# Performance work log

Measured on AMD Instinct MI355X. Metric: run time of the kernel, lower is better.

Reference implementation:

```python
import jax, jax.numpy as jnp
import numpy as np

B, D_IN, D_SAE = 4096, 1024, 16384
K_TOTAL = 262144  # B * 64 average active latents per sample


def setup_inputs() -> dict:
    key = jax.random.key(0)
    k1, k2, k3 = jax.random.split(key, 3)
    x = jax.random.normal(k1, (B, D_IN), dtype=jnp.float32)
    # torch kaiming_uniform_(a=sqrt(5)) on Linear weight -> bound = 1/sqrt(fan_in)
    bound_enc = 1.0 / np.sqrt(D_IN)
    W_enc = jax.random.uniform(k2, (D_IN, D_SAE), jnp.float32, -bound_enc, bound_enc)
    b_enc = jnp.zeros((D_SAE,), jnp.float32)
    bound_dec = 1.0 / np.sqrt(D_SAE)
    W_dec = jax.random.uniform(k3, (D_SAE, D_IN), jnp.float32, -bound_dec, bound_dec)
    b_dec = jnp.zeros((D_IN,), jnp.float32)
    return {"x": x, "W_enc": W_enc, "b_enc": b_enc,
            "W_dec": W_dec, "b_dec": b_dec, "k_total": K_TOTAL}


def reference(x, W_enc, b_enc, W_dec, b_dec, k_total):
    # encode: relu(x @ W_enc + b_enc), a: [B, M]
    a = jax.nn.relu(x @ W_enc + b_enc)
    Bn, M = a.shape
    # global batch top-k over the flattened activations, scatter back to sparse z
    flat = a.reshape(-1)                          # [B*M]
    vals, idx = jax.lax.top_k(flat, k_total)      # k_total is a static Python int
    z = jnp.zeros_like(flat).at[idx].set(vals).reshape(Bn, M)
    # decode
    x_hat = z @ W_dec + b_dec                     # [B, D_IN]
    # metrics (detached in torch; plain values here)
    nnz = (z > 0).sum()
    frac_nnz = nnz.astype(jnp.float32) / (Bn * M)
    mean_active = z.sum() / jnp.maximum(nnz.astype(jnp.float32), 1.0)
    return x_hat, z, frac_nnz, mean_active, nnz
```

## Files before the change

### kernel.cpp

```cpp
#include <hip/hip_runtime.h>
#include <stdint.h>

#define D_IN 1024
#define M_SAE 16384
#define NROWS 4096
#define NTOT 67108864
#define K_TOTAL 262144

#define META_OFF    0
#define GHIST_OFF   4096
#define ROWCNT_OFF  69632
#define PSUM_OFF    86016
#define CAND_OFF    102400
#define CAND_CAP    1048576
#define CAND2_OFF   8491008
#define CAND2_CAP   32768
#define ROWLIST_OFF 8753152
#define ROW_CAP     256
#define XBF_OFF     17141760
#define WBT_OFF     25530368

#define HBASE 7872u
#define HBINS 512
#define F_BITS 0x3FB00000u
#define FBIN   8152u
#define CBUF_CAP 1024

typedef __bf16 bf16x8 __attribute__((ext_vector_type(8)));
typedef float  f32x4  __attribute__((ext_vector_type(4)));

__device__ __forceinline__ unsigned short f2bf(float f) {
    uint32_t u = __float_as_uint(f);
    uint32_t r = u + 0x7FFFu + ((u >> 16) & 1u);
    return (unsigned short)(r >> 16);
}
__device__ __forceinline__ float bf2f(unsigned short s) {
    return __uint_as_float(((uint32_t)s) << 16);
}

__device__ __forceinline__ void load_lds16(const unsigned short* g, unsigned short* l) {
    __builtin_amdgcn_global_load_lds(
        (const __attribute__((address_space(1))) unsigned int*)g,
        (__attribute__((address_space(3))) unsigned int*)l, 16, 0, 0);
}

__global__ void conv_x(const float* __restrict__ in, unsigned short* __restrict__ out, int n4) {
    int i = blockIdx.x * blockDim.x + threadIdx.x;
    int stride = gridDim.x * blockDim.x;
    const float4* in4 = (const float4*)in;
    ushort4* out4 = (ushort4*)out;
    for (; i < n4; i += stride) {
        float4 v = in4[i];
        ushort4 o;
        o.x = f2bf(v.x); o.y = f2bf(v.y); o.z = f2bf(v.z); o.w = f2bf(v.w);
        out4[i] = o;
    }
}

__global__ __launch_bounds__(256) void conv_wT(const float* __restrict__ w,
                                               unsigned short* __restrict__ wT) {
    __shared__ unsigned short tile[64][65];
    int n0 = blockIdx.x * 64, k0 = blockIdx.y * 64;
    int c = threadIdx.x & 63;
    int r4 = threadIdx.x >> 6;
    #pragma unroll
    for (int rr = 0; rr < 16; rr++) {
        int kl = r4 * 16 + rr;
        tile[c][kl] = f2bf(w[(size_t)(k0 + kl) * M_SAE + n0 + c]);
    }
    __syncthreads();
    #pragma unroll
    for (int rr = 0; rr < 16; rr++) {
        int nl = r4 * 16 + rr;
        wT[(size_t)(n0 + nl) * D_IN + k0 + c] = tile[nl][c];
    }
}

__global__ void conv_wdec(const float* __restrict__ in, unsigned short* __restrict__ out) {
    int i = blockIdx.x * blockDim.x + threadIdx.x;
    const float4* in4 = (const float4*)in;
    ushort4* out4 = (ushort4*)out;
    float4 v = in4[i];
    ushort4 o;
    o.x = f2bf(v.x); o.y = f2bf(v.y); o.z = f2bf(v.z); o.w = f2bf(v.w);
    out4[i] = o;
}

__global__ __launch_bounds__(256) void gemm_encode(
    const unsigned short* __restrict__ xb,
    const unsigned short* __restrict__ wT,
    const float* __restrict__ be,
    float* __restrict__ aout,
    uint32_t* __restrict__ gh,
    uint32_t* __restrict__ meta,
    uint2* __restrict__ candg)
{
    __shared__ unsigned short As[128 * 32];
    __shared__ unsigned short Bs[128 * 32];
    __shared__ uint32_t hloc[HBINS];
    __shared__ uint2 cbuf[CBUF_CAP];
    __shared__ uint32_t ccnt, s_base, s_cn;
    const int tid  = threadIdx.x;
    const int lane = tid & 63;
    const int wv   = tid >> 6;
    const int wRow = (wv & 1) * 64;
    const int wCol = (wv >> 1) * 64;
    const int q    = lane >> 4;
    const int l16  = lane & 15;
    const int row0 = blockIdx.y * 128;
    const int col0 = blockIdx.x * 128;

    hloc[tid] = 0; hloc[tid + 256] = 0;
    if (tid == 0) ccnt = 0;

    const int rA0 = wv * 32 + (lane >> 2);
    const int rA1 = rA0 + 16;
    const int b0  = (lane & 3) ^ ((rA0 >> 1) & 3);
    const int b1  = (lane & 3) ^ ((rA1 >> 1) & 3);
    const unsigned short* gA0 = xb + (size_t)(row0 + rA0) * D_IN + b0 * 8;
    const unsigned short* gA1 = xb + (size_t)(row0 + rA1) * D_IN + b1 * 8;
    const unsigned short* gB0 = wT + (size_t)(col0 + rA0) * D_IN + b0 * 8;
    const unsigned short* gB1 = wT + (size_t)(col0 + rA1) * D_IN + b1 * 8;
    unsigned short* lA0 = &As[wv * 1024];
    unsigned short* lA1 = &As[wv * 1024 + 512];
    unsigned short* lB0 = &Bs[wv * 1024];
    unsigned short* lB1 = &Bs[wv * 1024 + 512];

    int offA[4], offB[4];
    #pragma unroll
    for (int i = 0; i < 4; i++) {
        int ra = wRow + 16 * i + l16;
        offA[i] = ra * 32 + (q ^ ((ra >> 1) & 3)) * 8;
        int rb = wCol + 16 * i + l16;
        offB[i] = rb * 32 + (q ^ ((rb >> 1) & 3)) * 8;
    }

    f32x4 acc[4][4];
    #pragma unroll
    for (int i = 0; i < 4; i++)
        #pragma unroll
        for (int j = 0; j < 4; j++) { f32x4 z = {0.f, 0.f, 0.f, 0.f}; acc[i][j] = z; }

    for (int k0 = 0; k0 < D_IN; k0 += 32) {
        load_lds16(gA0 + k0, lA0);
        load_lds16(gA1 + k0, lA1);
        load_lds16(gB0 + k0, lB0);
        load_lds16(gB1 + k0, lB1);
        __syncthreads();
        bf16x8 af[4], bfr[4];
        #pragma unroll
        for (int i = 0; i < 4; i++) af[i]  = *(const bf16x8*)&As[offA[i]];
        #pragma unroll
        for (int j = 0; j < 4; j++) bfr[j] = *(const bf16x8*)&Bs[offB[j]];
        #pragma unroll
        for (int i = 0; i < 4; i++)
            #pragma unroll
            for (int j = 0; j < 4; j++)
                acc[i][j] = __builtin_amdgcn_mfma_f32_16x16x32_bf16(af[i], bfr[j], acc[i][j], 0, 0, 0);
        __syncthreads();
    }
    #pragma unroll
    for (int i = 0; i < 4; i++) {
        #pragma unroll
        for (int j = 0; j < 4; j++) {
            int col = col0 + wCol + 16 * j + l16;
            float bias = be[col];
            #pragma unroll
            for (int r = 0; r < 4; r++) {
                int row = row0 + wRow + 16 * i + q * 4 + r;
                float v = acc[i][j][r] + bias;
                v = v > 0.f ? v : 0.f;
                aout[(size_t)row * M_SAE + col] = v;
                uint32_t u = __float_as_uint(v);
                if (u >= 0x3D800000u) {
                    uint32_t bin = (u >> 17) - HBASE;
                    if (bin > 511u) bin = 511u;
                    atomicAdd(&hloc[bin], 1u);
                    if (u >= F_BITS) {
                        uint32_t p = atomicAdd(&ccnt, 1u);
                        if (p < CBUF_CAP)
                            cbuf[p] = make_uint2((uint32_t)row * 16384u + (uint32_t)col, u);
                    }
                }
            }
        }
    }
    __syncthreads();
    {
        uint32_t c0 = hloc[tid], c1 = hloc[tid + 256];
        if (c0) atomicAdd(&gh[HBASE + tid], c0);
        if (c1) atomicAdd(&gh[HBASE + 256 + tid], c1);
    }
    if (tid == 0) {
        uint32_t cn = ccnt;
        if (cn > CBUF_CAP) { atomicExch(&meta[9], 1u); cn = CBUF_CAP; }
        s_base = atomicAdd(&meta[0], cn);
        s_cn = cn;
        if (s_base + cn > CAND_CAP) atomicExch(&meta[9], 1u);
    }
    __syncthreads();
    for (uint32_t i2 = tid; i2 < s_cn; i2 += 256) {
        uint32_t d = s_base + i2;
        if (d < CAND_CAP) candg[d] = cbuf[i2];
    }
}

__global__ __launch_bounds__(256) void find_bin(const uint32_t* __restrict__ gh,
                                                uint32_t* __restrict__ meta) {
    __shared__ uint32_t csum[256];
    __shared__ uint32_t pfx[257];
    int t = threadIdx.x;
    int hi = 16384 - 64 * t;
    uint32_t s = 0;
    for (int i = 0; i < 64; i++) s += gh[hi - 64 + i];
    csum[t] = s;
    __syncthreads();
    if (t == 0) {
        uint32_t c = 0;
        for (int i = 0; i < 256; i++) { pfx[i] = c; c += csum[i]; }
        pfx[256] = c;
    }
    __syncthreads();
    uint32_t above = pfx[t];
    if (above < K_TOTAL && above + csum[t] >= K_TOTAL) {
        uint32_t cum = above;
        for (int b = hi - 1; b >= hi - 64; b--) {
            uint32_t hh = gh[b];
            if (cum + hh >= K_TOTAL) {
                meta[1] = (uint32_t)b; meta[2] = cum;
                meta[7] = ((uint32_t)b >= FBIN && meta[9] == 0u) ? 1u : 0u;
                break;
            }
            cum += hh;
        }
    }
}

__global__ __launch_bounds__(256) void cand_scan(const uint2* __restrict__ cand,
                                                 uint32_t* __restrict__ meta,
                                                 uint32_t* __restrict__ rowcnt,
                                                 uint2* __restrict__ rowlist,
                                                 uint2* __restrict__ cand2,
                                                 float* __restrict__ psum) {
    if (meta[7] == 0u) return;
    __shared__ uint2 bbuf[256];
    __shared__ uint32_t bcnt, bbase, bn;
    __shared__ float wsum[4];
    const int tid = threadIdx.x;
    if (tid == 0) bcnt = 0;
    __syncthreads();
    uint32_t n = meta[0]; if (n > CAND_CAP) n = CAND_CAP;
    const uint32_t Bb = meta[1];
    const uint32_t TH = Bb << 17, TH2 = (Bb + 1) << 17;
    float lsum = 0.f;
    for (uint32_t i = blockIdx.x * 256 + tid; i < n; i += gridDim.x * 256) {
        uint2 cv = cand[i];
        if (cv.y >= TH2) {
            uint32_t gi = cv.x;
            uint32_t pos = atomicAdd(&rowcnt[gi >> 14], 1u);
            if (pos < ROW_CAP)
                rowlist[(size_t)(gi >> 14) * ROW_CAP + pos] =
                    make_uint2(gi & 16383u, cv.y);
            lsum += __uint_as_float(cv.y);
        } else if (cv.y >= TH) {
            uint32_t p = atomicAdd(&bcnt, 1u);
            if (p < 256u) bbuf[p] = cv;
        }
    }
    #pragma unroll
    for (int off = 32; off > 0; off >>= 1) lsum += __shfl_down(lsum, off);
    if ((tid & 63) == 0) wsum[tid >> 6] = lsum;
    __syncthreads();
    if (tid == 0) {
        psum[blockIdx.x] = wsum[0] + wsum[1] + wsum[2] + wsum[3];
        uint32_t cn = bcnt; if (cn > 256u) cn = 256u;
        bn = cn;
        bbase = cn ? atomicAdd(&meta[8], cn) : 0u;
    }
    __syncthreads();
    for (uint32_t i = tid; i < bn; i += 256) {
        uint32_t d = bbase + i;
        if (d < CAND2_CAP) cand2[d] = bbuf[i];
    }
}

__global__ __launch_bounds__(256) void scan_fallback(const uint4* __restrict__ z4,
                                                     uint32_t* __restrict__ meta,
                                                     uint32_t* __restrict__ rowcnt,
                                                     uint2* __restrict__ rowlist,
                                                     uint2* __restrict__ cand2,
                                                     float* __restrict__ psum) {
    if (meta[7] != 0u) return;
    __shared__ float wsum[4];
    const uint32_t Bb  = meta[1];
    const uint32_t TH  = Bb << 17;
    const uint32_t TH2 = (Bb + 1) << 17;
    const uint32_t t = blockIdx.x * 256 + threadIdx.x;
    const int lane = threadIdx.x & 63;
    float lsum = 0.f;
    for (int round = 0; round < 2; round++) {
        uint32_t i0 = (uint32_t)round * 8388608u + t;
        uint4 v[8];
        #pragma unroll
        for (int m = 0; m < 8; m++) v[m] = z4[i0 + m * 1048576u];

        uint2 c0v, c1v, c2v, c3v;
        int ccnt = 0;
        #pragma unroll
        for (int m = 0; m < 8; m++) {
            uint4 u = v[m];
            uint32_t mx = max(max(u.x, u.y), max(u.z, u.w));
            if (mx < TH) continue;
            uint32_t gbase = (i0 + m * 1048576u) * 4u;
            const uint32_t* vp = (const uint32_t*)&u;
            #pragma unroll
            for (int c = 0; c < 4; c++) {
                uint32_t b = vp[c];
                if (b >= TH2) {
                    uint32_t gi = gbase + (uint32_t)c;
                    uint32_t pos = atomicAdd(&rowcnt[gi >> 14], 1u);
                    if (pos < ROW_CAP)
                        rowlist[(size_t)(gi >> 14) * ROW_CAP + pos] =
                            make_uint2(gi & 16383u, b);
                    lsum += __uint_as_float(b);
                } else if (b >= TH) {
                    uint2 e = make_uint2(gbase + (uint32_t)c, b);
                    if (ccnt == 0) c0v = e; else if (ccnt == 1) c1v = e;
                    else if (ccnt == 2) c2v = e; else if (ccnt == 3) c3v = e;
                    ccnt++;
                }
            }
        }
        if (__ballot(ccnt != 0)) {
            int cc = ccnt > 4 ? 4 : ccnt;
            int incl = cc;
            #pragma unroll
            for (int off = 1; off < 64; off <<= 1) {
                int up = __shfl_up(incl, off);
                if (lane >= off) incl += up;
            }
            int total = __shfl(incl, 63);
            int base = 0;
            if (lane == 63 && total > 0) base = (int)atomicAdd(&meta[8], (uint32_t)total);
            base = __shfl(base, 63);
            uint32_t mb = (uint32_t)(base + incl - cc);
            if (cc > 0 && mb + 0 < CAND2_CAP) cand2[mb + 0] = c0v;
            if (cc > 1 && mb + 1 < CAND2_CAP) cand2[mb + 1] = c1v;
            if (cc > 2 && mb + 2 < CAND2_CAP) cand2[mb + 2] = c2v;
            if (cc > 3 && mb + 3 < CAND2_CAP) cand2[mb + 3] = c3v;
        }
    }
    #pragma unroll
    for (int off = 32; off > 0; off >>= 1) lsum += __shfl_down(lsum, off);
    if ((threadIdx.x & 63) == 0) wsum[threadIdx.x >> 6] = lsum;
    __syncthreads();
    if (threadIdx.x == 0) psum[blockIdx.x] = wsum[0] + wsum[1] + wsum[2] + wsum[3];
}

__global__ __launch_bounds__(1024) void refine_cutoff(const uint2* __restrict__ cand2,
                                                      uint32_t* __restrict__ meta,
                                                      uint32_t* __restrict__ rowcnt,
                                                      uint2* __restrict__ rowlist,
                                                      float* __restrict__ sum_out) {
    __shared__ uint32_t h1[512];
    __shared__ uint32_t h2[256];
    __shared__ uint32_t sS, scum2, tie_n;
    __shared__ uint32_t ties[64];
    int t = threadIdx.x;
    uint32_t n = meta[8]; if (n > CAND2_CAP) n = CAND2_CAP;
    uint32_t cum_above = meta[2];
    uint32_t Bb = meta[1];
    if (t < 512) h1[t] = 0;
    if (t < 256) h2[t] = 0;
    if (t == 0) tie_n = 0;
    __syncthreads();
    for (uint32_t i = t; i < n; i += 1024)
        atomicAdd(&h1[(cand2[i].y >> 8) & 511], 1u);
    __syncthreads();
    if (t == 0) {
        uint32_t cum = cum_above; uint32_t S = 0;
        for (int s = 511; s >= 0; s--) {
            if (cum + h1[s] >= K_TOTAL) { S = (uint32_t)s; break; }
            cum += h1[s];
        }
        sS = S; scum2 = cum;
    }
    __syncthreads();
    uint32_t S = sS;
    for (uint32_t i = t; i < n; i += 1024) {
        uint32_t bits = cand2[i].y;
        if (((bits >> 8) & 511) == S) atomicAdd(&h2[bits & 255], 1u);
    }
    __syncthreads();
    if (t == 0) {
        uint32_t cum = scum2; uint32_t L = 0;
        for (int l = 255; l >= 0; l--) {
            if (cum + h2[l] >= K_TOTAL) { L = (uint32_t)l; break; }
            cum += h2[l];
        }
        uint32_t cutoff = (Bb << 17) | (S << 8) | L;
        meta[3] = cutoff;
        meta[4] = cum;
        meta[5] = K_TOTAL - cum;
    }
    __syncthreads();
    uint32_t cutoff = meta[3];
    float lsum = 0.f;
    for (uint32_t i = t; i < n; i += 1024) {
        uint2 cv = cand2[i];
        if (cv.y > cutoff) {
            uint32_t gi = cv.x;
            uint32_t pos = atomicAdd(&rowcnt[gi >> 14], 1u);
            if (pos < ROW_CAP)
                rowlist[(size_t)(gi >> 14) * ROW_CAP + pos] =
                    make_uint2(gi & 16383u, cv.y);
            lsum += __uint_as_float(cv.y);
        } else if (cv.y == cutoff) {
            uint32_t p = atomicAdd(&tie_n, 1u);
            if (p < 64) ties[p] = cv.x;
        }
    }
    #pragma unroll
    for (int off = 32; off > 0; off >>= 1) lsum += __shfl_down(lsum, off);
    if ((t & 63) == 0 && lsum != 0.f) atomicAdd(sum_out, lsum);
    __syncthreads();
    if (t == 0) {
        uint32_t tn = tie_n; if (tn > 64) tn = 64;
        for (uint32_t i = 1; i < tn; i++) {
            uint32_t v = ties[i]; int j = (int)i - 1;
            while (j >= 0 && ties[j] > v) { ties[j + 1] = ties[j]; j--; }
            ties[j + 1] = v;
        }
        uint32_t need = meta[5]; if (need > tn) need = tn;
        meta[6] = need;
        float cv = __uint_as_float(cutoff);
        for (uint32_t i = 0; i < need; i++) {
            uint32_t gi = ties[i];
            uint32_t pos = atomicAdd(&rowcnt[gi >> 14], 1u);
            if (pos < ROW_CAP)
                rowlist[(size_t)(gi >> 14) * ROW_CAP + pos] =
                    make_uint2(gi & 16383u, cutoff);
        }
        if (need) atomicAdd(sum_out, cv * (float)need);
    }
}

__global__ __launch_bounds__(256) void decode(const uint32_t* __restrict__ rowcnt,
                                              const uint2* __restrict__ rowlist,
                                              const unsigned short* __restrict__ wdecb,
                                              const float* __restrict__ bdec,
                                              float* __restrict__ xhat,
                                              float* __restrict__ z) {
    __shared__ uint2 buf[256];
    int row = blockIdx.x;
    int t = threadIdx.x;
    uint32_t n = rowcnt[row]; if (n > ROW_CAP) n = ROW_CAP;
    float4 acc = *(const float4*)(bdec + t * 4);
    const uint2* lst = rowlist + (size_t)row * ROW_CAP;
    for (uint32_t base = 0; base < n; base += 256) {
        uint32_t m = n - base; if (m > 256) m = 256;
        __syncthreads();
        if ((uint32_t)t < m) {
            uint2 e = lst[base + t];
            buf[t] = e;
            z[(size_t)row * M_SAE + e.x] = __uint_as_float(e.y);
        }
        __syncthreads();
        uint32_t j = 0;
        for (; j + 4 <= m; j += 4) {
            uint2 p0 = buf[j], p1 = buf[j+1], p2 = buf[j+2], p3 = buf[j+3];
            ushort4 w0 = ((const ushort4*)(wdecb + (size_t)p0.x * D_IN))[t];
            ushort4 w1 = ((const ushort4*)(wdecb + (size_t)p1.x * D_IN))[t];
            ushort4 w2 = ((const ushort4*)(wdecb + (size_t)p2.x * D_IN))[t];
            ushort4 w3 = ((const ushort4*)(wdecb + (size_t)p3.x * D_IN))[t];
            float v0 = __uint_as_float(p0.y), v1 = __uint_as_float(p1.y);
            float v2 = __uint_as_float(p2.y), v3 = __uint_as_float(p3.y);
            acc.x += v0*bf2f(w0.x) + v1*bf2f(w1.x) + v2*bf2f(w2.x) + v3*bf2f(w3.x);
            acc.y += v0*bf2f(w0.y) + v1*bf2f(w1.y) + v2*bf2f(w2.y) + v3*bf2f(w3.y);
            acc.z += v0*bf2f(w0.z) + v1*bf2f(w1.z) + v2*bf2f(w2.z) + v3*bf2f(w3.z);
            acc.w += v0*bf2f(w0.w) + v1*bf2f(w1.w) + v2*bf2f(w2.w) + v3*bf2f(w3.w);
        }
        for (; j < m; j++) {
            uint2 p = buf[j];
            float val = __uint_as_float(p.y);
            ushort4 wv = ((const ushort4*)(wdecb + (size_t)p.x * D_IN))[t];
            acc.x += val * bf2f(wv.x); acc.y += val * bf2f(wv.y);
            acc.z += val * bf2f(wv.z); acc.w += val * bf2f(wv.w);
        }
    }
    *(float4*)(xhat + (size_t)row * D_IN + t * 4) = acc;
}

__global__ __launch_bounds__(1024) void scalars_kernel(const uint32_t* __restrict__ meta,
                                                       const float* __restrict__ psum,
                                                       float* __restrict__ out) {
    __shared__ float red[16];
    int t = threadIdx.x;
    float s = psum[t] + psum[t + 1024] + psum[t + 2048] + psum[t + 3072];
    #pragma unroll
    for (int off = 32; off > 0; off >>= 1) s += __shfl_down(s, off);
    if ((t & 63) == 0) red[t >> 6] = s;
    __syncthreads();
    if (t == 0) {
        float tot = ((const float*)meta)[72];
        #pragma unroll
        for (int i = 0; i < 16; i++) tot += red[i];
        uint32_t nnz = meta[4] + meta[6];
        out[0] = (float)nnz / (float)NTOT;
        out[1] = tot / fmaxf((float)nnz, 1.0f);
        out[2] = (float)nnz;
    }
}

extern "C" void kernel_launch(void* const* d_in, const int* in_sizes, int n_in,
                              void* d_out, int out_size, void* d_ws, size_t ws_size,
                              hipStream_t stream) {
    (void)in_sizes; (void)n_in; (void)out_size; (void)ws_size;
    const float* x     = (const float*)d_in[0];
    const float* W_enc = (const float*)d_in[1];
    const float* b_enc = (const float*)d_in[2];
    const float* W_dec = (const float*)d_in[3];
    const float* b_dec = (const float*)d_in[4];

    float* out  = (float*)d_out;
    float* xhat = out;
    float* z    = out + 4194304;
    float* scal = out + 4194304 + 67108864;

    uint8_t* ws = (uint8_t*)d_ws;
    uint32_t* meta     = (uint32_t*)(ws + META_OFF);
    uint32_t* ghist    = (uint32_t*)(ws + GHIST_OFF);
    uint32_t* rowcnt   = (uint32_t*)(ws + ROWCNT_OFF);
    float*    psum     = (float*)(ws + PSUM_OFF);
    uint2*    cand     = (uint2*)(ws + CAND_OFF);
    uint2*    cand2    = (uint2*)(ws + CAND2_OFF);
    uint2*    rowlist  = (uint2*)(ws + ROWLIST_OFF);
    unsigned short* xb = (unsigned short*)(ws + XBF_OFF);
    unsigned short* wT = (unsigned short*)(ws + WBT_OFF);

    hipMemsetAsync(ws, 0, 102400, stream);
    conv_x<<<1024, 256, 0, stream>>>(x, xb, 1048576);
    conv_wT<<<dim3(256, 16), 256, 0, stream>>>(W_enc, wT);
    gemm_encode<<<dim3(128, 32), 256, 0, stream>>>(xb, wT, b_enc, z, ghist, meta, cand);
    conv_wdec<<<16384, 256, 0, stream>>>(W_dec, wT);
    find_bin<<<1, 256, 0, stream>>>(ghist, meta);
    cand_scan<<<1024, 256, 0, stream>>>(cand, meta, rowcnt, rowlist, cand2, psum);
    scan_fallback<<<4096, 256, 0, stream>>>((const uint4*)z, meta, rowcnt, rowlist,
                                            cand2, psum);
    refine_cutoff<<<1, 1024, 0, stream>>>(cand2, meta, rowcnt, rowlist,
                                          (float*)(meta + 72));
    hipMemsetAsync(z, 0, (size_t)NTOT * 4, stream);
    decode<<<4096, 256, 0, stream>>>(rowcnt, rowlist, wT, b_dec, xhat, z);
    scalars_kernel<<<1, 1024, 0, stream>>>(meta, psum, scal);
}
```

Baseline: 804.0 us.

## Drop dense activation store from encode GEMM, recompute only on fallback path

The encode GEMM no longer writes the full 256MB dense activation matrix to z. It only builds the histogram and candidate list, and reuses the As/Bs shared memory for those buffers to cut LDS usage. A separate gemm_fallback kernel recomputes and stores the activations only when the candidate path fails (meta[7]==0). conv_wdec moves after the fallback so wT still holds the encoder weights. The cost is a full GEMM recompute on the rare fallback path, plus an extra kernel launch that exits early on the common path.

```diff
diff --git a/kernel.cpp b/kernel.cpp
--- a/kernel.cpp
+++ b/kernel.cpp
@@ -90,15 +90,12 @@
     const unsigned short* __restrict__ xb,
     const unsigned short* __restrict__ wT,
     const float* __restrict__ be,
-    float* __restrict__ aout,
     uint32_t* __restrict__ gh,
     uint32_t* __restrict__ meta,
     uint2* __restrict__ candg)
 {
-    __shared__ unsigned short As[128 * 32];
-    __shared__ unsigned short Bs[128 * 32];
-    __shared__ uint32_t hloc[HBINS];
-    __shared__ uint2 cbuf[CBUF_CAP];
+    __shared__ __attribute__((aligned(16))) unsigned short As[128 * 32];
+    __shared__ __attribute__((aligned(16))) unsigned short Bs[128 * 32];
     __shared__ uint32_t ccnt, s_base, s_cn;
     const int tid  = threadIdx.x;
     const int lane = tid & 63;
@@ -109,9 +106,6 @@
     const int l16  = lane & 15;
     const int row0 = blockIdx.y * 128;
     const int col0 = blockIdx.x * 128;
-
-    hloc[tid] = 0; hloc[tid + 256] = 0;
-    if (tid == 0) ccnt = 0;
 
     const int rA0 = wv * 32 + (lane >> 2);
     const int rA1 = rA0 + 16;
@@ -159,6 +153,13 @@
                 acc[i][j] = __builtin_amdgcn_mfma_f32_16x16x32_bf16(af[i], bfr[j], acc[i][j], 0, 0, 0);
         __syncthreads();
     }
+
+    uint2* cbuf = (uint2*)As;
+    uint32_t* hloc = (uint32_t*)Bs;
+    hloc[tid] = 0; hloc[tid + 256] = 0;
+    if (tid == 0) ccnt = 0;
+    __syncthreads();
+
     #pragma unroll
     for (int i = 0; i < 4; i++) {
         #pragma unroll
@@ -170,7 +171,6 @@
                 int row = row0 + wRow + 16 * i + q * 4 + r;
                 float v = acc[i][j][r] + bias;
                 v = v > 0.f ? v : 0.f;
-                aout[(size_t)row * M_SAE + col] = v;
                 uint32_t u = __float_as_uint(v);
                 if (u >= 0x3D800000u) {
                     uint32_t bin = (u >> 17) - HBASE;
@@ -281,6 +281,88 @@
     for (uint32_t i = tid; i < bn; i += 256) {
         uint32_t d = bbase + i;
         if (d < CAND2_CAP) cand2[d] = bbuf[i];
+    }
+}
+
+__global__ __launch_bounds__(256) void gemm_fallback(
+    const unsigned short* __restrict__ xb,
+    const unsigned short* __restrict__ wT,
+    const float* __restrict__ be,
+    float* __restrict__ aout,
+    const uint32_t* __restrict__ meta)
+{
+    if (meta[7] != 0u) return;
+    __shared__ __attribute__((aligned(16))) unsigned short As[128 * 32];
+    __shared__ __attribute__((aligned(16))) unsigned short Bs[128 * 32];
+    const int tid  = threadIdx.x;
+    const int lane = tid & 63;
+    const int wv   = tid >> 6;
+    const int wRow = (wv & 1) * 64;
+    const int wCol = (wv >> 1) * 64;
+    const int q    = lane >> 4;
+    const int l16  = lane & 15;
+    const int row0 = blockIdx.y * 128;
+    const int col0 = blockIdx.x * 128;
+
+    const int rA0 = wv * 32 + (lane >> 2);
+    const int rA1 = rA0 + 16;
+    const int b0  = (lane & 3) ^ ((rA0 >> 1) & 3);
+    const int b1  = (lane & 3) ^ ((rA1 >> 1) & 3);
+    const unsigned short* gA0 = xb + (size_t)(row0 + rA0) * D_IN + b0 * 8;
+    const unsigned short* gA1 = xb + (size_t)(row0 + rA1) * D_IN + b1 * 8;
+    const unsigned short* gB0 = wT + (size_t)(col0 + rA0) * D_IN + b0 * 8;
+    const unsigned short* gB1 = wT + (size_t)(col0 + rA1) * D_IN + b1 * 8;
+    unsigned short* lA0 = &As[wv * 1024];
+    unsigned short* lA1 = &As[wv * 1024 + 512];
+    unsigned short* lB0 = &Bs[wv * 1024];
+    unsigned short* lB1 = &Bs[wv * 1024 + 512];
+
+    int offA[4], offB[4];
+    #pragma unroll
+    for (int i = 0; i < 4; i++) {
+        int ra = wRow + 16 * i + l16;
+        offA[i] = ra * 32 + (q ^ ((ra >> 1) & 3)) * 8;
+        int rb = wCol + 16 * i + l16;
+        offB[i] = rb * 32 + (q ^ ((rb >> 1) & 3)) * 8;
+    }
+
+    f32x4 acc[4][4];
+    #pragma unroll
+    for (int i = 0; i < 4; i++)
+        #pragma unroll
+        for (int j = 0; j < 4; j++) { f32x4 z = {0.f, 0.f, 0.f, 0.f}; acc[i][j] = z; }
+
+    for (int k0 = 0; k0 < D_IN; k0 += 32) {
+        load_lds16(gA0 + k0, lA0);
+        load_lds16(gA1 + k0, lA1);
+        load_lds16(gB0 + k0, lB0);
+        load_lds16(gB1 + k0, lB1);
+        __syncthreads();
+        bf16x8 af[4], bfr[4];
+        #pragma unroll
+        for (int i = 0; i < 4; i++) af[i]  = *(const bf16x8*)&As[offA[i]];
+        #pragma unroll
+        for (int j = 0; j < 4; j++) bfr[j] = *(const bf16x8*)&Bs[offB[j]];
+        #pragma unroll
+        for (int i = 0; i < 4; i++)
+            #pragma unroll
+            for (int j = 0; j < 4; j++)
+                acc[i][j] = __builtin_amdgcn_mfma_f32_16x16x32_bf16(af[i], bfr[j], acc[i][j], 0, 0, 0);
+        __syncthreads();
+    }
+    #pragma unroll
+    for (int i = 0; i < 4; i++) {
+        #pragma unroll
+        for (int j = 0; j < 4; j++) {
+            int col = col0 + wCol + 16 * j + l16;
+            float bias = be[col];
+            #pragma unroll
+            for (int r = 0; r < 4; r++) {
+                int row = row0 + wRow + 16 * i + q * 4 + r;
+                float v = acc[i][j][r] + bias;
+                aout[(size_t)row * M_SAE + col] = v > 0.f ? v : 0.f;
+            }
+        }
     }
 }
 
@@ -541,12 +623,13 @@
     hipMemsetAsync(ws, 0, 102400, stream);
     conv_x<<<1024, 256, 0, stream>>>(x, xb, 1048576);
     conv_wT<<<dim3(256, 16), 256, 0, stream>>>(W_enc, wT);
-    gemm_encode<<<dim3(128, 32), 256, 0, stream>>>(xb, wT, b_enc, z, ghist, meta, cand);
-    conv_wdec<<<16384, 256, 0, stream>>>(W_dec, wT);
+    gemm_encode<<<dim3(128, 32), 256, 0, stream>>>(xb, wT, b_enc, ghist, meta, cand);
     find_bin<<<1, 256, 0, stream>>>(ghist, meta);
     cand_scan<<<1024, 256, 0, stream>>>(cand, meta, rowcnt, rowlist, cand2, psum);
+    gemm_fallback<<<dim3(128, 32), 256, 0, stream>>>(xb, wT, b_enc, z, meta);
     scan_fallback<<<4096, 256, 0, stream>>>((const uint4*)z, meta, rowcnt, rowlist,
                                             cand2, psum);
+    conv_wdec<<<16384, 256, 0, stream>>>(W_dec, wT);
     refine_cutoff<<<1, 1024, 0, stream>>>(cand2, meta, rowcnt, rowlist,
                                           (float*)(meta + 72));
     hipMemsetAsync(z, 0, (size_t)NTOT * 4, stream);
```

Result: no change. 793.9 us (-1.3%).

## Drop dense activation write from encode GEMM, add conditional fallback GEMM

Applied to the files above, without the earlier changes.

The encode GEMM no longer writes the full 4096x16384 fp32 activation matrix. It only builds the histogram and candidate list, and a separate fallback GEMM recomputes and stores activations only when the candidate path fails. The main GEMM also moves to 256x256 tiles with 512 threads, double-buffered LDS over K=64 steps, XCD-aware block mapping and setprio around the MFMAs. The W_dec conversion now runs after the fallback because it overwrites the wT buffer. This removes a 256MB store from the common path, at the cost of a much larger LDS footprint and duplicate GEMM work when the fallback triggers.

```diff
diff --git a/kernel.cpp b/kernel.cpp
--- a/kernel.cpp
+++ b/kernel.cpp
@@ -86,91 +86,126 @@
     out4[i] = o;
 }
 
-__global__ __launch_bounds__(256) void gemm_encode(
+__global__ __launch_bounds__(512, 2) void gemm_encode(
     const unsigned short* __restrict__ xb,
     const unsigned short* __restrict__ wT,
     const float* __restrict__ be,
-    float* __restrict__ aout,
     uint32_t* __restrict__ gh,
     uint32_t* __restrict__ meta,
     uint2* __restrict__ candg)
 {
-    __shared__ unsigned short As[128 * 32];
-    __shared__ unsigned short Bs[128 * 32];
-    __shared__ uint32_t hloc[HBINS];
-    __shared__ uint2 cbuf[CBUF_CAP];
+    __shared__ __attribute__((aligned(16))) unsigned short ldsbuf[65536];
     __shared__ uint32_t ccnt, s_base, s_cn;
+
     const int tid  = threadIdx.x;
     const int lane = tid & 63;
     const int wv   = tid >> 6;
-    const int wRow = (wv & 1) * 64;
-    const int wCol = (wv >> 1) * 64;
+    const int wm   = wv >> 2;
+    const int wn   = wv & 3;
     const int q    = lane >> 4;
     const int l16  = lane & 15;
-    const int row0 = blockIdx.y * 128;
-    const int col0 = blockIdx.x * 128;
-
-    hloc[tid] = 0; hloc[tid + 256] = 0;
+
+    const int bid = blockIdx.x;
+    const int xcd = bid & 7;
+    const int i8  = bid >> 3;
+    const int mT  = (xcd << 1) + (i8 >> 6);
+    const int nT  = i8 & 63;
+    const int row0 = mT * 256;
+    const int col0 = nT * 256;
+
+    const int r0 = tid >> 3;
+    const int sb = tid & 7;
+    const int bsrc = sb ^ (r0 & 7);
+    const unsigned short* pA = xb + (size_t)(row0 + r0) * D_IN + bsrc * 8;
+    const unsigned short* pB = wT + (size_t)(col0 + r0) * D_IN + bsrc * 8;
+
+    const int sx0 = ((0 * 4 + q) ^ (l16 & 7)) * 8;
+    const int sx1 = ((1 * 4 + q) ^ (l16 & 7)) * 8;
+    const int rowbaseA = (wm * 128 + l16) * 64;
+    const int rowbaseB = (wn * 64 + l16) * 64;
+
+    f32x4 acc[8][4];
+    #pragma unroll
+    for (int mi = 0; mi < 8; mi++)
+        #pragma unroll
+        for (int nj = 0; nj < 4; nj++) { f32x4 z = {0.f, 0.f, 0.f, 0.f}; acc[mi][nj] = z; }
+
+    {
+        unsigned short* nbA = &ldsbuf[0];
+        unsigned short* nbB = &ldsbuf[16384];
+        #pragma unroll
+        for (int a = 0; a < 4; a++) {
+            load_lds16(pA + a * 65536, nbA + a * 4096 + wv * 512);
+            load_lds16(pB + a * 65536, nbB + a * 4096 + wv * 512);
+        }
+    }
+    __syncthreads();
+
+    int cur = 0;
+    for (int kt = 0; kt < 16; kt++) {
+        const unsigned short* bufA = &ldsbuf[cur * 32768];
+        const unsigned short* bufB = bufA + 16384;
+        if (kt + 1 < 16) {
+            unsigned short* nbA = &ldsbuf[(cur ^ 1) * 32768];
+            unsigned short* nbB = nbA + 16384;
+            const int koff = (kt + 1) * 64;
+            #pragma unroll
+            for (int a = 0; a < 4; a++) {
+                load_lds16(pA + a * 65536 + koff, nbA + a * 4096 + wv * 512);
+                load_lds16(pB + a * 65536 + koff, nbB + a * 4096 + wv * 512);
+            }
+        }
+        bf16x8 bf[4][2];
+        #pragma unroll
+        for (int nj = 0; nj < 4; nj++) {
+            bf[nj][0] = *(const bf16x8*)&bufB[rowbaseB + nj * 1024 + sx0];
+            bf[nj][1] = *(const bf16x8*)&bufB[rowbaseB + nj * 1024 + sx1];
+        }
+        #pragma unroll
+        for (int p = 0; p < 4; p++) {
+            bf16x8 af0[2], af1[2];
+            #pragma unroll
+            for (int h = 0; h < 2; h++) {
+                int mi = 2 * p + h;
+                af0[h] = *(const bf16x8*)&bufA[rowbaseA + mi * 1024 + sx0];
+                af1[h] = *(const bf16x8*)&bufA[rowbaseA + mi * 1024 + sx1];
+            }
+            __builtin_amdgcn_s_setprio(1);
+            #pragma unroll
+            for (int h = 0; h < 2; h++) {
+                int mi = 2 * p + h;
+                #pragma unroll
+                for (int nj = 0; nj < 4; nj++) {
+                    acc[mi][nj] = __builtin_amdgcn_mfma_f32_16x16x32_bf16(af0[h], bf[nj][0], acc[mi][nj], 0, 0, 0);
+                    acc[mi][nj] = __builtin_amdgcn_mfma_f32_16x16x32_bf16(af1[h], bf[nj][1], acc[mi][nj], 0, 0, 0);
+                }
+            }
+            __builtin_amdgcn_s_setprio(0);
+        }
+        __syncthreads();
+        cur ^= 1;
+    }
+
+    uint32_t* hloc = (uint32_t*)&ldsbuf[0];
+    uint2* cbuf = (uint2*)&ldsbuf[2048];
+    hloc[tid] = 0;
     if (tid == 0) ccnt = 0;
-
-    const int rA0 = wv * 32 + (lane >> 2);
-    const int rA1 = rA0 + 16;
-    const int b0  = (lane & 3) ^ ((rA0 >> 1) & 3);
-    const int b1  = (lane & 3) ^ ((rA1 >> 1) & 3);
-    const unsigned short* gA0 = xb + (size_t)(row0 + rA0) * D_IN + b0 * 8;
-    const unsigned short* gA1 = xb + (size_t)(row0 + rA1) * D_IN + b1 * 8;
-    const unsigned short* gB0 = wT + (size_t)(col0 + rA0) * D_IN + b0 * 8;
-    const unsigned short* gB1 = wT + (size_t)(col0 + rA1) * D_IN + b1 * 8;
-    unsigned short* lA0 = &As[wv * 1024];
-    unsigned short* lA1 = &As[wv * 1024 + 512];
-    unsigned short* lB0 = &Bs[wv * 1024];
-    unsigned short* lB1 = &Bs[wv * 1024 + 512];
-
-    int offA[4], offB[4];
-    #pragma unroll
-    for (int i = 0; i < 4; i++) {
-        int ra = wRow + 16 * i + l16;
-        offA[i] = ra * 32 + (q ^ ((ra >> 1) & 3)) * 8;
-        int rb = wCol + 16 * i + l16;
-        offB[i] = rb * 32 + (q ^ ((rb >> 1) & 3)) * 8;
-    }
-
-    f32x4 acc[4][4];
-    #pragma unroll
-    for (int i = 0; i < 4; i++)
-        #pragma unroll
-        for (int j = 0; j < 4; j++) { f32x4 z = {0.f, 0.f, 0.f, 0.f}; acc[i][j] = z; }
-
-    for (int k0 = 0; k0 < D_IN; k0 += 32) {
-        load_lds16(gA0 + k0, lA0);
-        load_lds16(gA1 + k0, lA1);
-        load_lds16(gB0 + k0, lB0);
-        load_lds16(gB1 + k0, lB1);
-        __syncthreads();
-        bf16x8 af[4], bfr[4];
-        #pragma unroll
-        for (int i = 0; i < 4; i++) af[i]  = *(const bf16x8*)&As[offA[i]];
-        #pragma unroll
-        for (int j = 0; j < 4; j++) bfr[j] = *(const bf16x8*)&Bs[offB[j]];
-        #pragma unroll
-        for (int i = 0; i < 4; i++)
-            #pragma unroll
-            for (int j = 0; j < 4; j++)
-                acc[i][j] = __builtin_amdgcn_mfma_f32_16x16x32_bf16(af[i], bfr[j], acc[i][j], 0, 0, 0);
-        __syncthreads();
-    }
-    #pragma unroll
-    for (int i = 0; i < 4; i++) {
-        #pragma unroll
-        for (int j = 0; j < 4; j++) {
-            int col = col0 + wCol + 16 * j + l16;
-            float bias = be[col];
-            #pragma unroll
-            for (int r = 0; r < 4; r++) {
-                int row = row0 + wRow + 16 * i + q * 4 + r;
-                float v = acc[i][j][r] + bias;
+    __syncthreads();
+
+    float bias_n[4];
+    #pragma unroll
+    for (int nj = 0; nj < 4; nj++) bias_n[nj] = be[col0 + wn * 64 + nj * 16 + l16];
+
+    #pragma unroll
+    for (int mi = 0; mi < 8; mi++) {
+        #pragma unroll
+        for (int nj = 0; nj < 4; nj++) {
+            int col = col0 + wn * 64 + nj * 16 + l16;
+            #pragma unroll
+            for (int rr = 0; rr < 4; rr++) {
+                int row = row0 + wm * 128 + mi * 16 + q * 4 + rr;
+                float v = acc[mi][nj][rr] + bias_n[nj];
                 v = v > 0.f ? v : 0.f;
-                aout[(size_t)row * M_SAE + col] = v;
                 uint32_t u = __float_as_uint(v);
                 if (u >= 0x3D800000u) {
                     uint32_t bin = (u >> 17) - HBASE;
@@ -187,9 +222,8 @@
     }
     __syncthreads();
     {
-        uint32_t c0 = hloc[tid], c1 = hloc[tid + 256];
+        uint32_t c0 = hloc[tid];
         if (c0) atomicAdd(&gh[HBASE + tid], c0);
-        if (c1) atomicAdd(&gh[HBASE + 256 + tid], c1);
     }
     if (tid == 0) {
         uint32_t cn = ccnt;
@@ -199,7 +233,7 @@
         if (s_base + cn > CAND_CAP) atomicExch(&meta[9], 1u);
     }
     __syncthreads();
-    for (uint32_t i2 = tid; i2 < s_cn; i2 += 256) {
+    for (uint32_t i2 = tid; i2 < s_cn; i2 += 512) {
         uint32_t d = s_base + i2;
         if (d < CAND_CAP) candg[d] = cbuf[i2];
     }
@@ -281,6 +315,88 @@
     for (uint32_t i = tid; i < bn; i += 256) {
         uint32_t d = bbase + i;
         if (d < CAND2_CAP) cand2[d] = bbuf[i];
+    }
+}
+
+__global__ __launch_bounds__(256) void gemm_fallback(
+    const unsigned short* __restrict__ xb,
+    const unsigned short* __restrict__ wT,
+    const float* __restrict__ be,
+    float* __restrict__ aout,
+    const uint32_t* __restrict__ meta)
+{
+    if (meta[7] != 0u) return;
+    __shared__ __attribute__((aligned(16))) unsigned short As[128 * 32];
+    __shared__ __attribute__((aligned(16))) unsigned short Bs[128 * 32];
+    const int tid  = threadIdx.x;
+    const int lane = tid & 63;
+    const int wv   = tid >> 6;
+    const int wRow = (wv & 1) * 64;
+    const int wCol = (wv >> 1) * 64;
+    const int q    = lane >> 4;
+    const int l16  = lane & 15;
+    const int row0 = blockIdx.y * 128;
+    const int col0 = blockIdx.x * 128;
+
+    const int rA0 = wv * 32 + (lane >> 2);
+    const int rA1 = rA0 + 16;
+    const int b0  = (lane & 3) ^ ((rA0 >> 1) & 3);
+    const int b1  = (lane & 3) ^ ((rA1 >> 1) & 3);
+    const unsigned short* gA0 = xb + (size_t)(row0 + rA0) * D_IN + b0 * 8;
+    const unsigned short* gA1 = xb + (size_t)(row0 + rA1) * D_IN + b1 * 8;
+    const unsigned short* gB0 = wT + (size_t)(col0 + rA0) * D_IN + b0 * 8;
+    const unsigned short* gB1 = wT + (size_t)(col0 + rA1) * D_IN + b1 * 8;
+    unsigned short* lA0 = &As[wv * 1024];
+    unsigned short* lA1 = &As[wv * 1024 + 512];
+    unsigned short* lB0 = &Bs[wv * 1024];
+    unsigned short* lB1 = &Bs[wv * 1024 + 512];
+
+    int offA[4], offB[4];
+    #pragma unroll
+    for (int i = 0; i < 4; i++) {
+        int ra = wRow + 16 * i + l16;
+        offA[i] = ra * 32 + (q ^ ((ra >> 1) & 3)) * 8;
+        int rb = wCol + 16 * i + l16;
+        offB[i] = rb * 32 + (q ^ ((rb >> 1) & 3)) * 8;
+    }
+
+    f32x4 acc[4][4];
+    #pragma unroll
+    for (int i = 0; i < 4; i++)
+        #pragma unroll
+        for (int j = 0; j < 4; j++) { f32x4 z = {0.f, 0.f, 0.f, 0.f}; acc[i][j] = z; }
+
+    for (int k0 = 0; k0 < D_IN; k0 += 32) {
+        load_lds16(gA0 + k0, lA0);
+        load_lds16(gA1 + k0, lA1);
+        load_lds16(gB0 + k0, lB0);
+        load_lds16(gB1 + k0, lB1);
+        __syncthreads();
+        bf16x8 af[4], bfr[4];
+        #pragma unroll
+        for (int i = 0; i < 4; i++) af[i]  = *(const bf16x8*)&As[offA[i]];
+        #pragma unroll
+        for (int j = 0; j < 4; j++) bfr[j] = *(const bf16x8*)&Bs[offB[j]];
+        #pragma unroll
+        for (int i = 0; i < 4; i++)
+            #pragma unroll
+            for (int j = 0; j < 4; j++)
+                acc[i][j] = __builtin_amdgcn_mfma_f32_16x16x32_bf16(af[i], bfr[j], acc[i][j], 0, 0, 0);
+        __syncthreads();
+    }
+    #pragma unroll
+    for (int i = 0; i < 4; i++) {
+        #pragma unroll
+        for (int j = 0; j < 4; j++) {
+            int col = col0 + wCol + 16 * j + l16;
+            float bias = be[col];
+            #pragma unroll
+            for (int r = 0; r < 4; r++) {
+                int row = row0 + wRow + 16 * i + q * 4 + r;
+                float v = acc[i][j][r] + bias;
+                aout[(size_t)row * M_SAE + col] = v > 0.f ? v : 0.f;
+            }
+        }
     }
 }
 
@@ -541,12 +657,13 @@
     hipMemsetAsync(ws, 0, 102400, stream);
     conv_x<<<1024, 256, 0, stream>>>(x, xb, 1048576);
     conv_wT<<<dim3(256, 16), 256, 0, stream>>>(W_enc, wT);
-    gemm_encode<<<dim3(128, 32), 256, 0, stream>>>(xb, wT, b_enc, z, ghist, meta, cand);
-    conv_wdec<<<16384, 256, 0, stream>>>(W_dec, wT);
+    gemm_encode<<<1024, 512, 0, stream>>>(xb, wT, b_enc, ghist, meta, cand);
     find_bin<<<1, 256, 0, stream>>>(ghist, meta);
     cand_scan<<<1024, 256, 0, stream>>>(cand, meta, rowcnt, rowlist, cand2, psum);
+    gemm_fallback<<<dim3(128, 32), 256, 0, stream>>>(xb, wT, b_enc, z, meta);
     scan_fallback<<<4096, 256, 0, stream>>>((const uint4*)z, meta, rowcnt, rowlist,
                                             cand2, psum);
+    conv_wdec<<<16384, 256, 0, stream>>>(W_dec, wT);
     refine_cutoff<<<1, 1024, 0, stream>>>(cand2, meta, rowcnt, rowlist,
                                           (float*)(meta + 72));
     hipMemsetAsync(z, 0, (size_t)NTOT * 4, stream);
```

Result: faster. 758.3 us (-5.7%).
